# Optimization experiments

Hardware: AMD Instinct MI355X
Metric: run time of the kernel (lower is better)

The kernel has to match this reference:

```python
import jax, jax.numpy as jnp
import numpy as np

DIM = 256
B, W_IN, H_IN = 8, 96, 96


def setup_inputs() -> dict:
    key = jax.random.key(0)
    k1, k2, k3 = jax.random.split(key, 3)
    x = jax.random.normal(k1, (B, W_IN, H_IN, DIM), dtype=jnp.float32)
    # Conv2d(dim, 3*dim, kernel_size=1): weight (3C, C) (1x1 spatial dropped), bias (3C,)
    w_qkv = jax.random.normal(k2, (3 * DIM, DIM), dtype=jnp.float32) * (1.0 / np.sqrt(DIM))
    b_qkv = jax.random.normal(k3, (3 * DIM,), dtype=jnp.float32) * 0.01
    return {"x": x, "w_qkv": w_qkv, "b_qkv": b_qkv}


def reference(x, w_qkv, b_qkv):
    # x: (B, W, H, C) -> transpose(3,1) -> (B, C, H, W)
    xt = jnp.transpose(x, (0, 3, 2, 1))
    # 1x1 conv == channel GEMM
    qvk = jnp.einsum('bchw,oc->bohw', xt, w_qkv) + b_qkv[None, :, None, None]
    q, k, v = jnp.split(qvk, 3, axis=1)  # each (B, C, H, W)
    Bn, C, H, W = q.shape

    q_t = jnp.transpose(q, (0, 2, 1, 3))            # (B, H, C, W)
    qk = q_t.reshape(Bn, H * C, W)                   # (B, H*C, W)
    qf = q_t.reshape(Bn, H, C * W)                   # (B, H, C*W)
    kq = jnp.transpose(k, (0, 1, 3, 2)).reshape(Bn, C * W, H)  # (B, C*W, H)
    ms = jax.nn.softmax(jnp.matmul(qf, kq), axis=-1)  # (B, H, H) attention over H

    kf = jnp.transpose(k, (0, 3, 2, 1)).reshape(Bn, W, H * C)  # (B, W, H*C)
    ma = jax.nn.softmax(jnp.matmul(kf, qk), axis=-1)  # (B, W, W) attention over W

    vq = jnp.transpose(v, (0, 2, 1, 3)).reshape(Bn, H, C * W)  # (B, H, C*W)
    vk = jnp.transpose(v, (0, 3, 2, 1)).reshape(Bn, W, H * C)  # (B, W, H*C)

    ms = jnp.matmul(ms, vq).reshape(Bn, H, C, W)     # view(B, H, C, W)
    ms = jnp.transpose(ms, (0, 2, 1, 3))             # (B, C, H, W)
    ma = jnp.matmul(ma, vk).reshape(Bn, W, H, C)     # view(B, W, H, C)
    ma = jnp.transpose(ma, (0, 3, 2, 1))             # (B, C, H, W)

    # final transpose(3,1): (B, C, H, W) -> (B, W, H, C)
    return jnp.transpose(ms + ma, (0, 3, 2, 1))
```

## Files before the change

kernel.cpp:

```cpp
#include <hip/hip_runtime.h>
#include <math.h>

#define SQ 96
#define CQ 256
#define OQ 768
#define HWQ 9216
#define PIXQ 73728

typedef __attribute__((ext_vector_type(8))) __bf16 bf16x8;
typedef __attribute__((ext_vector_type(4))) float f32x4;

union FragU { uint4 u; bf16x8 b; };

__device__ inline uint32_t bf16_rne_u(float f) {
  uint32_t u = __float_as_uint(f);
  return (u + 0x7FFFu + ((u >> 16) & 1u)) >> 16;
}
__device__ inline uint32_t pack_split(float f) {
  uint32_t hi = bf16_rne_u(f);
  float rem = f - __uint_as_float(hi << 16);
  uint32_t lo = __float_as_uint(rem) >> 16;
  return hi | (lo << 16);
}
__device__ inline void unpack_frags(uint4 r0, uint4 r1, FragU& hi, FragU& lo) {
  hi.u.x = (r0.x & 0xFFFFu) | (r0.y << 16);
  hi.u.y = (r0.z & 0xFFFFu) | (r0.w << 16);
  hi.u.z = (r1.x & 0xFFFFu) | (r1.y << 16);
  hi.u.w = (r1.z & 0xFFFFu) | (r1.w << 16);
  lo.u.x = (r0.x >> 16) | (r0.y & 0xFFFF0000u);
  lo.u.y = (r0.z >> 16) | (r0.w & 0xFFFF0000u);
  lo.u.z = (r1.x >> 16) | (r1.y & 0xFFFF0000u);
  lo.u.w = (r1.z >> 16) | (r1.w & 0xFFFF0000u);
}

__device__ inline uint32_t* swz(uint32_t* base, int row, int colb) {
  return base + row * 32 + ((colb ^ ((row & 7) << 4)) >> 2);
}
__device__ inline const uint32_t* swzc(const uint32_t* base, int row, int colb) {
  return base + row * 32 + ((colb ^ ((row & 7) << 4)) >> 2);
}

__global__ __launch_bounds__(256) void pack_w_kernel(
    const float* __restrict__ w, uint32_t* __restrict__ wp) {
  int i = blockIdx.x * 256 + threadIdx.x;
  wp[i] = pack_split(w[i]);
}

__global__ __launch_bounds__(256) void qkv_gemm_mfma(
    const float* __restrict__ x, const uint32_t* __restrict__ wp,
    const float* __restrict__ bias, uint32_t* __restrict__ qk,
    ushort* __restrict__ vb) {
  __shared__ uint32_t Apk[128 * 32];
  __shared__ uint32_t Bpk[128 * 32];
  const int tid = threadIdx.x;
  const int lane = tid & 63;
  const int wid = tid >> 6;
  const int wm = wid >> 1, wn = wid & 1;
  const int lr = lane & 15, quad = lane >> 4;
  const int lin = (blockIdx.x & 7) * 432 + (blockIdx.x >> 3);
  const int m0 = (lin / 6) * 128, n0 = (lin % 6) * 128;
  const int sr = tid >> 1, skh = (tid & 1) * 16;

  f32x4 acc[4][4] = {};

  for (int k0 = 0; k0 < 256; k0 += 32) {
    const float* xsrc = x + (size_t)(m0 + sr) * 256 + k0 + skh;
#pragma unroll
    for (int j = 0; j < 4; ++j) {
      float4 v = *(const float4*)(xsrc + 4 * j);
      uint4 p;
      p.x = pack_split(v.x); p.y = pack_split(v.y);
      p.z = pack_split(v.z); p.w = pack_split(v.w);
      *(uint4*)swz(Apk, sr, skh * 4 + j * 16) = p;
    }
    const uint32_t* wsrc = wp + (size_t)(n0 + sr) * 256 + k0 + skh;
#pragma unroll
    for (int j = 0; j < 4; ++j)
      *(uint4*)swz(Bpk, sr, skh * 4 + j * 16) = *(const uint4*)(wsrc + 4 * j);
    __syncthreads();

    FragU ah[4], al[4], bh[4], bl[4];
#pragma unroll
    for (int t = 0; t < 4; ++t) {
      const int ra = wm * 64 + t * 16 + lr;
      unpack_frags(*(const uint4*)swzc(Apk, ra, quad * 32),
                   *(const uint4*)swzc(Apk, ra, quad * 32 + 16), ah[t], al[t]);
      const int rb = wn * 64 + t * 16 + lr;
      unpack_frags(*(const uint4*)swzc(Bpk, rb, quad * 32),
                   *(const uint4*)swzc(Bpk, rb, quad * 32 + 16), bh[t], bl[t]);
    }
#pragma unroll
    for (int i = 0; i < 4; ++i)
#pragma unroll
      for (int j = 0; j < 4; ++j) {
        acc[i][j] = __builtin_amdgcn_mfma_f32_16x16x32_bf16(al[i].b, bh[j].b, acc[i][j], 0, 0, 0);
        acc[i][j] = __builtin_amdgcn_mfma_f32_16x16x32_bf16(ah[i].b, bl[j].b, acc[i][j], 0, 0, 0);
        acc[i][j] = __builtin_amdgcn_mfma_f32_16x16x32_bf16(ah[i].b, bh[j].b, acc[i][j], 0, 0, 0);
      }
    __syncthreads();
  }

#pragma unroll
  for (int i = 0; i < 4; ++i) {
    const int growb = m0 + wm * 64 + i * 16 + quad * 4;
#pragma unroll
    for (int r = 0; r < 4; ++r) {
      int p = growb + r;
      int b = p / HWQ;
      int rem = p - b * HWQ;
      int ww = rem / SQ;
      int hh = rem - ww * SQ;
      size_t opix = (size_t)b * HWQ + (size_t)hh * SQ + ww;
#pragma unroll
      for (int j = 0; j < 4; ++j) {
        int o = n0 + wn * 64 + j * 16 + lr;
        float val = acc[i][j][r] + bias[o];
        if (o < 512) qk[opix * 512 + o] = pack_split(val);
        else vb[opix * 256 + (o - 512)] = (ushort)bf16_rne_u(val);
      }
    }
  }
}

__global__ __launch_bounds__(256) void attn_scores_mfma(
    const uint32_t* __restrict__ qk, float* __restrict__ Sh,
    float* __restrict__ Sw) {
  __shared__ uint32_t Xpk[96 * 32];
  __shared__ uint32_t Ypk[96 * 32];
  const int tid = threadIdx.x;
  const int lane = tid & 63;
  const int wid = tid >> 6;
  const int wm = wid >> 1, wn = wid & 1;
  const int lr = lane & 15, quad = lane >> 4;
  const int chunk = blockIdx.x;
  const int b = blockIdx.y;
  const int which = blockIdx.z;
  const size_t base = (size_t)b * HWQ * 512;
  const int offX = which ? 256 : 0;
  const int offY = which ? 0 : 256;

  f32x4 acc[3][3] = {};

  for (int it = 0; it < 24; ++it) {
    int kout = chunk * 3 + (it >> 3);
    int c0 = (it & 7) * 32;
#pragma unroll
    for (int j = 0; j < 3; ++j) {
      int s = j * 256 + tid;
      int row = s >> 3;
      int colb = (s & 7) * 16;
      size_t idx = which ? ((size_t)kout * SQ + row) : ((size_t)row * SQ + kout);
      const uint32_t* src = qk + base + idx * 512 + c0 + (colb >> 2);
      *(uint4*)swz(Xpk, row, colb) = *(const uint4*)(src + offX);
      *(uint4*)swz(Ypk, row, colb) = *(const uint4*)(src + offY);
    }
    __syncthreads();
    FragU xh[3], xl[3], yh[3], yl[3];
#pragma unroll
    for (int t = 0; t < 3; ++t) {
      const int rx = wm * 48 + t * 16 + lr;
      unpack_frags(*(const uint4*)swzc(Xpk, rx, quad * 32),
                   *(const uint4*)swzc(Xpk, rx, quad * 32 + 16), xh[t], xl[t]);
      const int ry = wn * 48 + t * 16 + lr;
      unpack_frags(*(const uint4*)swzc(Ypk, ry, quad * 32),
                   *(const uint4*)swzc(Ypk, ry, quad * 32 + 16), yh[t], yl[t]);
    }
#pragma unroll
    for (int i = 0; i < 3; ++i)
#pragma unroll
      for (int j = 0; j < 3; ++j) {
        acc[i][j] = __builtin_amdgcn_mfma_f32_16x16x32_bf16(xl[i].b, yh[j].b, acc[i][j], 0, 0, 0);
        acc[i][j] = __builtin_amdgcn_mfma_f32_16x16x32_bf16(xh[i].b, yl[j].b, acc[i][j], 0, 0, 0);
        acc[i][j] = __builtin_amdgcn_mfma_f32_16x16x32_bf16(xh[i].b, yh[j].b, acc[i][j], 0, 0, 0);
      }
    __syncthreads();
  }
  float* S = which ? Sw : Sh;
#pragma unroll
  for (int i = 0; i < 3; ++i)
#pragma unroll
    for (int r = 0; r < 4; ++r)
#pragma unroll
      for (int j = 0; j < 3; ++j) {
        int row = wm * 48 + i * 16 + quad * 4 + r;
        int col = wn * 48 + j * 16 + lr;
        atomicAdd(S + ((size_t)b * SQ + row) * SQ + col, acc[i][j][r]);
      }
}

__global__ __launch_bounds__(256) void softmax_p(
    const float* __restrict__ Sh, const float* __restrict__ Sw,
    ushort* __restrict__ Pms, ushort* __restrict__ Pma) {
  const int tid = threadIdx.x;
  const int lane = tid & 63;
  const int row = blockIdx.x * 4 + (tid >> 6);
  const float* p = (row < 768) ? (Sh + (size_t)row * SQ)
                               : (Sw + (size_t)(row - 768) * SQ);
  ushort* q = (row < 768) ? (Pms + (size_t)row * SQ)
                          : (Pma + (size_t)(row - 768) * SQ);
  float v0 = p[lane];
  float v1 = (lane < 32) ? p[64 + lane] : -3.0e38f;
  float m = fmaxf(v0, v1);
#pragma unroll
  for (int off = 32; off > 0; off >>= 1) m = fmaxf(m, __shfl_xor(m, off));
  float e0 = __expf(v0 - m);
  float e1 = (lane < 32) ? __expf(v1 - m) : 0.0f;
  float s = e0 + e1;
#pragma unroll
  for (int off = 32; off > 0; off >>= 1) s += __shfl_xor(s, off);
  float inv = 1.0f / s;
  q[lane] = (ushort)bf16_rne_u(e0 * inv);
  if (lane < 32) q[64 + lane] = (ushort)bf16_rne_u(e1 * inv);
}

__global__ __launch_bounds__(256) void attn_apply_mfma(
    const ushort* __restrict__ vb, const ushort* __restrict__ P,
    float* __restrict__ out, const int which) {
  __shared__ ushort Vt[256 * 40];
  const int tid = threadIdx.x;
  const int lane = tid & 63;
  const int wid = tid >> 6;
  const int wm = wid >> 1, wn = wid & 1;
  const int lr = lane & 15, quad = lane >> 4;
  const int xi = blockIdx.x;
  const int b = blockIdx.y;

  f32x4 acc[3][8] = {};

  for (int k0 = 0; k0 < 96; k0 += 32) {
#pragma unroll
    for (int j = 0; j < 8; ++j) {
      int bi = j * 256 + tid;
      int c2 = bi & 127;
      int k2 = bi >> 7;
      int k = k0 + k2 * 2;
      int c = c2 * 2;
      size_t r0, r1;
      if (which == 0) {
        r0 = ((size_t)b * HWQ + (size_t)k * SQ + xi) * CQ + c;
        r1 = r0 + (size_t)SQ * CQ;
      } else {
        r0 = ((size_t)b * HWQ + (size_t)xi * SQ + k) * CQ + c;
        r1 = r0 + CQ;
      }
      uint32_t a0 = *(const uint32_t*)(vb + r0);
      uint32_t a1 = *(const uint32_t*)(vb + r1);
      uint32_t w0 = (a0 & 0xFFFFu) | (a1 << 16);
      uint32_t w1 = (a0 >> 16) | (a1 & 0xFFFF0000u);
      *(uint32_t*)&Vt[c * 40 + k2 * 2] = w0;
      *(uint32_t*)&Vt[(c + 1) * 40 + k2 * 2] = w1;
    }
    __syncthreads();
    FragU a[3];
#pragma unroll
    for (int t = 0; t < 3; ++t) {
      int row = wm * 48 + t * 16 + lr;
      const ushort* ps = P + ((size_t)b * SQ + row) * SQ + k0 + quad * 8;
      a[t].u = *(const uint4*)ps;
    }
#pragma unroll
    for (int j = 0; j < 8; ++j) {
      int cb = wn * 128 + j * 16 + lr;
      FragU bf;
      bf.u = *(const uint4*)&Vt[cb * 40 + quad * 8];
#pragma unroll
      for (int i = 0; i < 3; ++i)
        acc[i][j] = __builtin_amdgcn_mfma_f32_16x16x32_bf16(a[i].b, bf.b, acc[i][j], 0, 0, 0);
    }
    __syncthreads();
  }

#pragma unroll
  for (int i = 0; i < 3; ++i) {
#pragma unroll
    for (int r = 0; r < 4; ++r) {
      int mrow = wm * 48 + i * 16 + quad * 4 + r;
      size_t obase;
      if (which == 0) obase = (((size_t)b * SQ + xi) * SQ + mrow) * CQ;
      else            obase = (((size_t)b * SQ + mrow) * SQ + xi) * CQ;
#pragma unroll
      for (int j = 0; j < 8; ++j) {
        int c = wn * 128 + j * 16 + lr;
        if (which == 0) out[obase + c] = acc[i][j][r];
        else            out[obase + c] += acc[i][j][r];
      }
    }
  }
}

extern "C" void kernel_launch(void* const* d_in, const int* in_sizes, int n_in,
                              void* d_out, int out_size, void* d_ws,
                              size_t ws_size, hipStream_t stream) {
  const float* x = (const float*)d_in[0];
  const float* w = (const float*)d_in[1];
  const float* bias = (const float*)d_in[2];
  float* out = (float*)d_out;

  uint32_t* qk  = (uint32_t*)d_ws;
  ushort*   vb  = (ushort*)(qk + (size_t)PIXQ * 512);
  float*    Sh  = (float*)(vb + (size_t)PIXQ * 256);
  float*    Sw  = Sh + PIXQ;
  ushort*   Pms = (ushort*)(Sw + PIXQ);
  ushort*   Pma = Pms + PIXQ;
  uint32_t* wp  = (uint32_t*)(Pma + PIXQ);

  hipMemsetAsync(Sh, 0, 2 * (size_t)PIXQ * sizeof(float), stream);

  pack_w_kernel<<<dim3(768), 256, 0, stream>>>(w, wp);
  qkv_gemm_mfma<<<dim3(3456), 256, 0, stream>>>(x, wp, bias, qk, vb);
  attn_scores_mfma<<<dim3(32, 8, 2), 256, 0, stream>>>(qk, Sh, Sw);
  softmax_p<<<dim3(384), 256, 0, stream>>>(Sh, Sw, Pms, Pma);
  attn_apply_mfma<<<dim3(96, 8), 256, 0, stream>>>(vb, Pms, out, 0);
  attn_apply_mfma<<<dim3(96, 8), 256, 0, stream>>>(vb, Pma, out, 1);
}
```

Before: 453.0 us.

## Pre-split inputs into swizzled hi/lo tiles and load LDS via global_load_lds

A new pre-pass splits x and W into bf16 hi/lo planes, laid out in pre-swizzled 32-wide K tiles, and writes them to scratch (x goes into the output buffer). Both MFMA kernels then fill LDS with direct global-to-LDS 16-byte DMA and read hi/lo fragments with no unpack step. The q/k intermediates are stored as separate hi and lo ushort planes, and the scores kernel picks a plane per DMA chunk. This removes in-kernel conversion and register staging. The cost is an extra full pass over x and scattered 2-byte stores in the GEMM epilogue.

```diff
diff --git a/kernel.cpp b/kernel.cpp
--- a/kernel.cpp
+++ b/kernel.cpp
@@ -22,34 +22,47 @@
   uint32_t lo = __float_as_uint(rem) >> 16;
   return hi | (lo << 16);
 }
-__device__ inline void unpack_frags(uint4 r0, uint4 r1, FragU& hi, FragU& lo) {
-  hi.u.x = (r0.x & 0xFFFFu) | (r0.y << 16);
-  hi.u.y = (r0.z & 0xFFFFu) | (r0.w << 16);
-  hi.u.z = (r1.x & 0xFFFFu) | (r1.y << 16);
-  hi.u.w = (r1.z & 0xFFFFu) | (r1.w << 16);
-  lo.u.x = (r0.x >> 16) | (r0.y & 0xFFFF0000u);
-  lo.u.y = (r0.z >> 16) | (r0.w & 0xFFFF0000u);
-  lo.u.z = (r1.x >> 16) | (r1.y & 0xFFFF0000u);
-  lo.u.w = (r1.z >> 16) | (r1.w & 0xFFFF0000u);
-}
-
-__device__ inline uint32_t* swz(uint32_t* base, int row, int colb) {
-  return base + row * 32 + ((colb ^ ((row & 7) << 4)) >> 2);
-}
+
 __device__ inline const uint32_t* swzc(const uint32_t* base, int row, int colb) {
   return base + row * 32 + ((colb ^ ((row & 7) << 4)) >> 2);
 }
 
-__global__ __launch_bounds__(256) void pack_w_kernel(
-    const float* __restrict__ w, uint32_t* __restrict__ wp) {
-  int i = blockIdx.x * 256 + threadIdx.x;
-  wp[i] = pack_split(w[i]);
+__device__ inline void lds_dma16(const void* g, void* l) {
+  __builtin_amdgcn_global_load_lds(
+      (const __attribute__((address_space(1))) uint32_t*)g,
+      (__attribute__((address_space(3))) uint32_t*)l, 16, 0, 0);
+}
+
+__global__ __launch_bounds__(256) void split_tiles_kernel(
+    const float* __restrict__ src, uint32_t* __restrict__ dst) {
+  int t = blockIdx.x * 256 + threadIdx.x;
+  int e = t * 8;
+  int m = e >> 8;
+  int rem = e & 255;
+  int kc = rem >> 5;
+  int k8 = (rem & 31) >> 3;
+  const float* s = src + (size_t)m * 256 + rem;
+  uint32_t h[4], l[4];
+#pragma unroll
+  for (int i = 0; i < 2; ++i) {
+    float4 v = *(const float4*)(s + 4 * i);
+    uint32_t p0 = pack_split(v.x), p1 = pack_split(v.y);
+    uint32_t p2 = pack_split(v.z), p3 = pack_split(v.w);
+    h[2 * i]     = (p0 & 0xFFFFu) | (p1 << 16);
+    h[2 * i + 1] = (p2 & 0xFFFFu) | (p3 << 16);
+    l[2 * i]     = (p0 >> 16) | (p1 & 0xFFFF0000u);
+    l[2 * i + 1] = (p2 >> 16) | (p3 & 0xFFFF0000u);
+  }
+  int swz = (m & 7) << 4;
+  uint32_t* rowp = dst + ((size_t)m * 8 + kc) * 32;
+  *(uint4*)(rowp + (((k8 * 16) ^ swz) >> 2)) = *(uint4*)h;
+  *(uint4*)(rowp + (((64 + k8 * 16) ^ swz) >> 2)) = *(uint4*)l;
 }
 
 __global__ __launch_bounds__(256) void qkv_gemm_mfma(
-    const float* __restrict__ x, const uint32_t* __restrict__ wp,
-    const float* __restrict__ bias, uint32_t* __restrict__ qk,
-    ushort* __restrict__ vb) {
+    const uint32_t* __restrict__ xps, const uint32_t* __restrict__ wps,
+    const float* __restrict__ bias, ushort* __restrict__ qkh,
+    ushort* __restrict__ qkl, ushort* __restrict__ vb) {
   __shared__ uint32_t Apk[128 * 32];
   __shared__ uint32_t Bpk[128 * 32];
   const int tid = threadIdx.x;
@@ -59,35 +72,31 @@
   const int lr = lane & 15, quad = lane >> 4;
   const int lin = (blockIdx.x & 7) * 432 + (blockIdx.x >> 3);
   const int m0 = (lin / 6) * 128, n0 = (lin % 6) * 128;
-  const int sr = tid >> 1, skh = (tid & 1) * 16;
+  const int srow = tid >> 3;
+  const int scol = (tid & 7) * 4;
 
   f32x4 acc[4][4] = {};
 
-  for (int k0 = 0; k0 < 256; k0 += 32) {
-    const float* xsrc = x + (size_t)(m0 + sr) * 256 + k0 + skh;
+  const uint32_t* aP = xps + (size_t)(m0 + srow) * 256 + scol;
+  const uint32_t* bP = wps + (size_t)(n0 + srow) * 256 + scol;
+
+  for (int kc = 0; kc < 8; ++kc) {
 #pragma unroll
     for (int j = 0; j < 4; ++j) {
-      float4 v = *(const float4*)(xsrc + 4 * j);
-      uint4 p;
-      p.x = pack_split(v.x); p.y = pack_split(v.y);
-      p.z = pack_split(v.z); p.w = pack_split(v.w);
-      *(uint4*)swz(Apk, sr, skh * 4 + j * 16) = p;
-    }
-    const uint32_t* wsrc = wp + (size_t)(n0 + sr) * 256 + k0 + skh;
-#pragma unroll
-    for (int j = 0; j < 4; ++j)
-      *(uint4*)swz(Bpk, sr, skh * 4 + j * 16) = *(const uint4*)(wsrc + 4 * j);
+      lds_dma16(aP + j * 8192 + kc * 32, &Apk[j * 1024 + tid * 4]);
+      lds_dma16(bP + j * 8192 + kc * 32, &Bpk[j * 1024 + tid * 4]);
+    }
     __syncthreads();
 
     FragU ah[4], al[4], bh[4], bl[4];
 #pragma unroll
     for (int t = 0; t < 4; ++t) {
       const int ra = wm * 64 + t * 16 + lr;
-      unpack_frags(*(const uint4*)swzc(Apk, ra, quad * 32),
-                   *(const uint4*)swzc(Apk, ra, quad * 32 + 16), ah[t], al[t]);
+      ah[t].u = *(const uint4*)swzc(Apk, ra, quad * 16);
+      al[t].u = *(const uint4*)swzc(Apk, ra, 64 + quad * 16);
       const int rb = wn * 64 + t * 16 + lr;
-      unpack_frags(*(const uint4*)swzc(Bpk, rb, quad * 32),
-                   *(const uint4*)swzc(Bpk, rb, quad * 32 + 16), bh[t], bl[t]);
+      bh[t].u = *(const uint4*)swzc(Bpk, rb, quad * 16);
+      bl[t].u = *(const uint4*)swzc(Bpk, rb, 64 + quad * 16);
     }
 #pragma unroll
     for (int i = 0; i < 4; ++i)
@@ -115,16 +124,21 @@
       for (int j = 0; j < 4; ++j) {
         int o = n0 + wn * 64 + j * 16 + lr;
         float val = acc[i][j][r] + bias[o];
-        if (o < 512) qk[opix * 512 + o] = pack_split(val);
-        else vb[opix * 256 + (o - 512)] = (ushort)bf16_rne_u(val);
+        if (o < 512) {
+          uint32_t ps = pack_split(val);
+          qkh[opix * 512 + o] = (ushort)ps;
+          qkl[opix * 512 + o] = (ushort)(ps >> 16);
+        } else {
+          vb[opix * 256 + (o - 512)] = (ushort)bf16_rne_u(val);
+        }
       }
     }
   }
 }
 
 __global__ __launch_bounds__(256) void attn_scores_mfma(
-    const uint32_t* __restrict__ qk, float* __restrict__ Sh,
-    float* __restrict__ Sw) {
+    const ushort* __restrict__ qkh, const ushort* __restrict__ qkl,
+    float* __restrict__ Sh, float* __restrict__ Sw) {
   __shared__ uint32_t Xpk[96 * 32];
   __shared__ uint32_t Ypk[96 * 32];
   const int tid = threadIdx.x;
@@ -138,6 +152,8 @@
   const size_t base = (size_t)b * HWQ * 512;
   const int offX = which ? 256 : 0;
   const int offY = which ? 0 : 256;
+  const int srow = tid >> 3;
+  const int byteoff = (tid & 7) * 16;
 
   f32x4 acc[3][3] = {};
 
@@ -146,24 +162,27 @@
     int c0 = (it & 7) * 32;
 #pragma unroll
     for (int j = 0; j < 3; ++j) {
-      int s = j * 256 + tid;
-      int row = s >> 3;
-      int colb = (s & 7) * 16;
-      size_t idx = which ? ((size_t)kout * SQ + row) : ((size_t)row * SQ + kout);
-      const uint32_t* src = qk + base + idx * 512 + c0 + (colb >> 2);
-      *(uint4*)swz(Xpk, row, colb) = *(const uint4*)(src + offX);
-      *(uint4*)swz(Ypk, row, colb) = *(const uint4*)(src + offY);
-    }
-    __syncthreads();
+      int row = j * 32 + srow;
+      int nom = byteoff ^ ((row & 7) << 4);
+      const ushort* plane = (nom & 64) ? qkl : qkh;
+      int within = (nom & 63) >> 1;
+      size_t pix = which ? ((size_t)kout * SQ + row) : ((size_t)row * SQ + kout);
+      const ushort* sX = plane + base + pix * 512 + offX + c0 + within;
+      const ushort* sY = plane + base + pix * 512 + offY + c0 + within;
+      lds_dma16(sX, &Xpk[j * 1024 + tid * 4]);
+      lds_dma16(sY, &Ypk[j * 1024 + tid * 4]);
+    }
+    __syncthreads();
+
     FragU xh[3], xl[3], yh[3], yl[3];
 #pragma unroll
     for (int t = 0; t < 3; ++t) {
       const int rx = wm * 48 + t * 16 + lr;
-      unpack_frags(*(const uint4*)swzc(Xpk, rx, quad * 32),
-                   *(const uint4*)swzc(Xpk, rx, quad * 32 + 16), xh[t], xl[t]);
+      xh[t].u = *(const uint4*)swzc(Xpk, rx, quad * 16);
+      xl[t].u = *(const uint4*)swzc(Xpk, rx, 64 + quad * 16);
       const int ry = wn * 48 + t * 16 + lr;
-      unpack_frags(*(const uint4*)swzc(Ypk, ry, quad * 32),
-                   *(const uint4*)swzc(Ypk, ry, quad * 32 + 16), yh[t], yl[t]);
+      yh[t].u = *(const uint4*)swzc(Ypk, ry, quad * 16);
+      yl[t].u = *(const uint4*)swzc(Ypk, ry, 64 + quad * 16);
     }
 #pragma unroll
     for (int i = 0; i < 3; ++i)
@@ -296,19 +315,23 @@
   const float* bias = (const float*)d_in[2];
   float* out = (float*)d_out;
 
-  uint32_t* qk  = (uint32_t*)d_ws;
-  ushort*   vb  = (ushort*)(qk + (size_t)PIXQ * 512);
-  float*    Sh  = (float*)(vb + (size_t)PIXQ * 256);
-  float*    Sw  = Sh + PIXQ;
-  ushort*   Pms = (ushort*)(Sw + PIXQ);
-  ushort*   Pma = Pms + PIXQ;
-  uint32_t* wp  = (uint32_t*)(Pma + PIXQ);
+  ushort* qkh = (ushort*)d_ws;
+  ushort* qkl = qkh + (size_t)PIXQ * 512;
+  ushort* vb  = qkl + (size_t)PIXQ * 512;
+  float*  Sh  = (float*)(vb + (size_t)PIXQ * 256);
+  float*  Sw  = Sh + PIXQ;
+  ushort* Pms = (ushort*)(Sw + PIXQ);
+  ushort* Pma = Pms + PIXQ;
+  uint32_t* wps = (uint32_t*)(Pma + PIXQ);
+
+  uint32_t* xps = (uint32_t*)d_out;
 
   hipMemsetAsync(Sh, 0, 2 * (size_t)PIXQ * sizeof(float), stream);
 
-  pack_w_kernel<<<dim3(768), 256, 0, stream>>>(w, wp);
-  qkv_gemm_mfma<<<dim3(3456), 256, 0, stream>>>(x, wp, bias, qk, vb);
-  attn_scores_mfma<<<dim3(32, 8, 2), 256, 0, stream>>>(qk, Sh, Sw);
+  split_tiles_kernel<<<dim3(9216), 256, 0, stream>>>(x, xps);
+  split_tiles_kernel<<<dim3(96), 256, 0, stream>>>(w, wps);
+  qkv_gemm_mfma<<<dim3(3456), 256, 0, stream>>>(xps, wps, bias, qkh, qkl, vb);
+  attn_scores_mfma<<<dim3(32, 8, 2), 256, 0, stream>>>(qkh, qkl, Sh, Sw);
   softmax_p<<<dim3(384), 256, 0, stream>>>(Sh, Sw, Pms, Pma);
   attn_apply_mfma<<<dim3(96, 8), 256, 0, stream>>>(vb, Pms, out, 0);
   attn_apply_mfma<<<dim3(96, 8), 256, 0, stream>>>(vb, Pma, out, 1);
```

New measurement: 418.6 us. 1.08x faster.
